# Performance work log

Hardware: AMD Instinct MI355X
Metric: run time of the kernel (lower is better)

The kernel has to match this reference:

```python
import jax, jax.numpy as jnp
import numpy as np

N, D, DFF, E, K = 2048, 1024, 4096, 8, 2  # tokens, d_model, d_ff, num_expert, top_k


def setup_inputs() -> dict:
    key = jax.random.key(0)
    ks = jax.random.split(key, 5)
    s = 0.02  # init scale
    return {
        "moe_inp": jax.random.normal(ks[0], (N, D), jnp.float32),
        "Wg": jax.random.normal(ks[1], (D, E), jnp.float32) * s,   # gate linear
        "bg": jnp.zeros((E,), jnp.float32),
        "W1": jax.random.normal(ks[2], (E, D, DFF), jnp.float32) * s,  # htoh4 per expert
        "b1": jnp.zeros((E, DFF), jnp.float32),
        "W2": jax.random.normal(ks[3], (E, DFF, D), jnp.float32) * s,  # h4toh per expert
        "b2": jnp.zeros((E, D), jnp.float32),
    }


def reference(moe_inp, Wg, bg, W1, b1, W2, b2):
    # --- NaiveGate: top-k experts per token, softmax over selected logits ---
    logits = moe_inp @ Wg + bg                      # [N, E]
    top_val, top_idx = jax.lax.top_k(logits, K)     # [N, K]
    score = jax.nn.softmax(top_val, axis=-1)        # [N, K]

    # Dense combine weights c[n, e] = sum_j score[n, j] * 1{top_idx[n, j] == e}.
    # This is the mathematically exact equivalent of scatter -> grouped expert
    # GEMM -> gather -> score-weighted combine in fmoe.
    comb = jnp.einsum(
        "nke,nk->ne", jax.nn.one_hot(top_idx, E, dtype=moe_inp.dtype), score
    )                                               # [N, E]

    # --- per-expert FFN: relu(x W1 + b1) W2 + b2, masked-combined by comb ---
    h = jax.nn.relu(jnp.einsum("nd,edh->enh", moe_inp, W1) + b1[:, None, :])  # [E, N, DFF]
    out = jnp.einsum("enh,ehd,ne->nd", h, W2, comb) + comb @ b2               # [N, D]
    return out
```

## Files before the change

kernel.cpp:

```cpp
#include <hip/hip_runtime.h>
#include <hip/hip_bf16.h>
#include <cstdint>
#include <cstddef>

#define NTOKS  2048
#define DMODEL 1024
#define DFFN   4096
#define NEXP   8
#define TS128  40

typedef __attribute__((ext_vector_type(8))) short short8;
typedef __attribute__((ext_vector_type(4))) float f32x4;
typedef __attribute__((ext_vector_type(4))) unsigned short u16x4;
typedef __attribute__((ext_vector_type(8))) unsigned short u16x8;

static constexpr size_t alignup(size_t x) { return (x + 255) & ~(size_t)255; }
static constexpr size_t OFF_XB   = 0;
static constexpr size_t OFF_CNT  = alignup(OFF_XB + (size_t)(NTOKS + 1) * DMODEL * 2);
static constexpr size_t OFF_OFFS = OFF_CNT + 256;
static constexpr size_t OFF_TOKE = OFF_OFFS + 256;
static constexpr size_t OFF_TOKT = OFF_TOKE + (size_t)NTOKS * 2 * 4;
static constexpr size_t OFF_TOKS = OFF_TOKT + (size_t)NTOKS * 2 * 4;
static constexpr size_t OFF_TI2  = alignup(OFF_TOKS + (size_t)NTOKS * 2 * 4);
static constexpr size_t OFF_CAP  = alignup(OFF_TI2 + TS128 * 8);
static constexpr size_t OFF_H    = alignup(OFF_CAP + (size_t)NEXP * NTOKS * 4);
static constexpr size_t OFF_WBA  = alignup(OFF_H + (size_t)(NTOKS * 2 + 128) * DFFN * 2);
static constexpr size_t OFF_WBB  = alignup(OFF_WBA + (size_t)NEXP * DMODEL * DFFN * 2);
static constexpr size_t OFF_Y    = OFF_WBA;

__device__ inline unsigned short f2bf(float f) {
  __hip_bfloat16 h = __float2bfloat16(f);
  return __builtin_bit_cast(unsigned short, h);
}

__device__ inline void gload16(const void* g, void* l) {
  __builtin_amdgcn_global_load_lds((const __attribute__((address_space(1))) unsigned int*)g,
                                   (__attribute__((address_space(3))) unsigned int*)l, 16, 0, 0);
}


__device__ __forceinline__ void conv_body(const float* __restrict__ x,
                                          unsigned short* __restrict__ xb, int vb) {
  size_t base = ((size_t)vb * 256 + threadIdx.x) * 8;
  const size_t total = (size_t)(NTOKS + 1) * DMODEL;
  if (base >= total) return;
  u16x8 o;
  if (base < (size_t)NTOKS * DMODEL) {
    f32x4 a = *(const f32x4*)(x + base);
    f32x4 b = *(const f32x4*)(x + base + 4);
#pragma unroll
    for (int j = 0; j < 4; ++j) { o[j] = f2bf(a[j]); o[4 + j] = f2bf(b[j]); }
  } else {
#pragma unroll
    for (int j = 0; j < 8; ++j) o[j] = 0;
  }
  *(u16x8*)(xb + base) = o;
}

template <int R, int C>
__device__ __forceinline__ void tc_body(const float* __restrict__ W,
                                        unsigned short* __restrict__ WT,
                                        int bx, int by, int bz,
                                        unsigned short (*T)[66]) {
  const int e = bz;
  const int c0 = bx * 64, r0 = by * 64;
  const float* Wp = W + (size_t)e * R * C;
  unsigned short* Tp = WT + (size_t)e * R * C;
  const int tid = threadIdx.x;
  const int rr = tid >> 4, cc = (tid & 15) << 2;
#pragma unroll
  for (int i = 0; i < 4; ++i) {
    int r = rr + (i << 4);
    f32x4 v = *(const f32x4*)(Wp + (size_t)(r0 + r) * C + c0 + cc);
    T[r][cc]     = f2bf(v[0]);
    T[r][cc + 1] = f2bf(v[1]);
    T[r][cc + 2] = f2bf(v[2]);
    T[r][cc + 3] = f2bf(v[3]);
  }
  __syncthreads();
  const int c = tid >> 2, kc = (tid & 3) << 4;
  u16x8 o0, o1;
#pragma unroll
  for (int i = 0; i < 8; ++i) { o0[i] = T[kc + i][c]; o1[i] = T[kc + 8 + i][c]; }
  unsigned short* dst = Tp + (size_t)(c0 + c) * R + r0 + kc;
  *(u16x8*)(dst) = o0;
  *(u16x8*)(dst + 8) = o1;
}

__device__ __forceinline__ void gate_body(const float* __restrict__ x,
                                          const float* __restrict__ Wg,
                                          const float* __restrict__ bg,
                                          int* __restrict__ tok_e,
                                          float* __restrict__ tok_s, int vb) {
  const int w = threadIdx.x >> 6, lane = threadIdx.x & 63;
  const int n = vb * 4 + w;
  float acc[8];
#pragma unroll
  for (int e = 0; e < 8; ++e) acc[e] = 0.f;
  const float* xr = x + (size_t)n * DMODEL;
#pragma unroll 4
  for (int it = 0; it < DMODEL / 64; ++it) {
    int d = it * 64 + lane;
    float xv = xr[d];
    f32x4 w0 = *(const f32x4*)(Wg + d * 8);
    f32x4 w1 = *(const f32x4*)(Wg + d * 8 + 4);
#pragma unroll
    for (int j = 0; j < 4; ++j) { acc[j] += xv * w0[j]; acc[4 + j] += xv * w1[j]; }
  }
#pragma unroll
  for (int e = 0; e < 8; ++e)
#pragma unroll
    for (int off = 32; off; off >>= 1) acc[e] += __shfl_xor(acc[e], off, 64);
  if (lane == 0) {
    float l[8];
#pragma unroll
    for (int e = 0; e < 8; ++e) l[e] = acc[e] + bg[e];
    int i0 = 0; float v0 = l[0];
#pragma unroll
    for (int e = 1; e < 8; ++e) if (l[e] > v0) { v0 = l[e]; i0 = e; }
    int i1 = (i0 == 0) ? 1 : 0; float v1 = l[i1];
#pragma unroll
    for (int e = 0; e < 8; ++e) if (e != i0 && l[e] > v1) { v1 = l[e]; i1 = e; }
    float t = expf(v1 - v0);
    float inv = 1.f / (1.f + t);
    tok_e[2 * n] = i0; tok_e[2 * n + 1] = i1;
    tok_s[2 * n] = inv; tok_s[2 * n + 1] = t * inv;
  }
}

template <int KTOT, int NTOT, int BN, bool FIRST, int KSPLIT>
__device__ __forceinline__ void gemm_body(const unsigned short* __restrict__ Asrc,
                                          const unsigned short* __restrict__ Bsrc,
                                          const float* __restrict__ bias,
                                          const int* __restrict__ cnt,
                                          const int* __restrict__ offs,
                                          const int2* __restrict__ tinfo,
                                          const int* __restrict__ cap,
                                          unsigned short* __restrict__ hout,
                                          float* __restrict__ yout,
                                          int bx, int by, int bz, char* smem) {
  const int2 ti = tinfo[by];
  if (ti.x < 0) return;
  const int e = ti.x, t0 = ti.y;
  const int c = cnt[e];
  const int base = offs[e] + t0;
  const int n0 = bx * BN;
  constexpr int KCH = KTOT / KSPLIT;
  constexpr int NT = KCH / 32;
  const int kb = bz * KCH;

  const int tid = threadIdx.x, w = tid >> 6, lane = tid & 63;
  const int l15 = lane & 15, lq = lane >> 4;
  constexpr int MR = 4;
  constexpr int NR = BN / 32;
  constexpr int BR = BN / 64;
  const int wr = w >> 1, wc = w & 1;

  unsigned short (*As)[128 * 32] = (unsigned short (*)[128 * 32])smem;
  unsigned short (*Bs)[BN * 32]  = (unsigned short (*)[BN * 32])(smem + 2 * 128 * 32 * 2);

  const int rl = tid >> 2;
  const int sw = (((tid & 3) ^ (rl & 3) ^ ((rl >> 2) & 3)) << 3);
  const unsigned short* aptr[2];
#pragma unroll
  for (int r = 0; r < 2; ++r) {
    int row = r * 64 + rl;
    size_t gr;
    if constexpr (FIRST) gr = (size_t)((t0 + row < c) ? cap[e * NTOKS + t0 + row] : NTOKS);
    else                 gr = (size_t)(base + row);
    aptr[r] = Asrc + gr * (size_t)KTOT + kb + sw;
  }
  const unsigned short* Be = Bsrc + (size_t)e * ((size_t)KTOT * NTOT);
  const unsigned short* bptr[BR];
#pragma unroll
  for (int r = 0; r < BR; ++r)
    bptr[r] = Be + (size_t)(n0 + r * 64 + rl) * KTOT + kb + sw;

  auto stageA = [&](int k0, int b) {
#pragma unroll
    for (int r = 0; r < 2; ++r)
      gload16(aptr[r] + k0, &As[b][(r * 64 + w * 16) << 5]);
  };
  auto stageB = [&](int k0, int b) {
#pragma unroll
    for (int r = 0; r < BR; ++r)
      gload16(bptr[r] + k0, &Bs[b][(r * 64 + w * 16) << 5]);
  };

  f32x4 acc[MR][NR] = {};

  stageA(0, 0);
  stageB(0, 0);
  __syncthreads();

  int buf = 0;
  for (int t = 0; t < NT; ++t) {
    const int nxt = buf ^ 1;
    if (t + 1 < NT) { stageA((t + 1) * 32, nxt); stageB((t + 1) * 32, nxt); }

    short8 a[MR], b[NR];
    const int sw0 = ((lq ^ (l15 & 3) ^ ((l15 >> 2) & 3)) << 3);
#pragma unroll
    for (int m = 0; m < MR; ++m)
      a[m] = *(const short8*)&As[buf][((wr * 64 + m * 16 + l15) << 5) + sw0];
#pragma unroll
    for (int nn = 0; nn < NR; ++nn)
      b[nn] = *(const short8*)&Bs[buf][((wc * (BN / 2) + nn * 16 + l15) << 5) + sw0];
#pragma unroll
    for (int m = 0; m < MR; ++m)
#pragma unroll
      for (int nn = 0; nn < NR; ++nn)
        acc[m][nn] = __builtin_amdgcn_mfma_f32_16x16x32_bf16(a[m], b[nn], acc[m][nn], 0, 0, 0);

    __syncthreads();
    buf = nxt;
  }

  if constexpr (FIRST) {
    const float* be = bias + (size_t)e * NTOT;
#pragma unroll
    for (int m = 0; m < MR; ++m) {
#pragma unroll
      for (int q2 = 0; q2 < 4; ++q2) {
        int row = wr * 64 + m * 16 + lq * 4 + q2;
        if (t0 + row < c) {
          unsigned short* hr = hout + (size_t)(base + row) * NTOT;
#pragma unroll
          for (int nn = 0; nn < NR; ++nn) {
            int col = n0 + wc * (BN / 2) + nn * 16 + l15;
            float v = acc[m][nn][q2] + be[col];
            v = v > 0.f ? v : 0.f;
            hr[col] = f2bf(v);
          }
        }
      }
    }
  } else {
    float* yz = yout + (size_t)bz * NTOKS * 2 * DMODEL;
#pragma unroll
    for (int m = 0; m < MR; ++m) {
#pragma unroll
      for (int q2 = 0; q2 < 4; ++q2) {
        int row = wr * 64 + m * 16 + lq * 4 + q2;
        if (t0 + row < c) {
          float* yr = yz + (size_t)(base + row) * NTOT;
#pragma unroll
          for (int nn = 0; nn < NR; ++nn) {
            int col = n0 + wc * (BN / 2) + nn * 16 + l15;
            yr[col] = acc[m][nn][q2];
          }
        }
      }
    }
  }
}


__global__ __launch_bounds__(256) void k_phase1(const float* __restrict__ x,
                                                const float* __restrict__ Wg,
                                                const float* __restrict__ bg,
                                                const float* __restrict__ W1,
                                                unsigned short* __restrict__ xb,
                                                unsigned short* __restrict__ wbA,
                                                int* __restrict__ tok_e,
                                                float* __restrict__ tok_s) {
  __shared__ unsigned short T[64][66];
  constexpr int NTC1 = (DFFN / 64) * (DMODEL / 64) * NEXP;
  constexpr int NCV  = (int)(((size_t)(NTOKS + 1) * DMODEL / 8 + 255) / 256);
  const int b = blockIdx.x;
  if (b < NTC1) {
    const int bx = b & 63, by = (b >> 6) & 15, bz = b >> 10;
    tc_body<DMODEL, DFFN>(W1, wbA, bx, by, bz, T);
  } else if (b < NTC1 + NCV) {
    conv_body(x, xb, b - NTC1);
  } else {
    gate_body(x, Wg, bg, tok_e, tok_s, b - NTC1 - NCV);
  }
}

__global__ __launch_bounds__(512) void k_scan(const int* __restrict__ tok_e,
                                              int* __restrict__ cnt,
                                              int* __restrict__ offs,
                                              int* __restrict__ tok_t,
                                              int* __restrict__ cap,
                                              int2* __restrict__ ti128) {
  __shared__ int scnt[NEXP];
  const int w = threadIdx.x >> 6, lane = threadIdx.x & 63;
  if (w < NEXP) {
    const int e = w;
    int t = 0;
    for (int it = 0; it < (NTOKS * 2) / 64; ++it) {
      const int j = it * 64 + lane;
      const bool p = (tok_e[j] == e);
      const unsigned long long m = __ballot(p);
      const int pos = __popcll(m & ((1ull << lane) - 1ull));
      if (p) {
        cap[e * NTOKS + t + pos] = j >> 1;
        tok_t[j] = t + pos;
      }
      t += __popcll(m);
    }
    if (lane == 0) { scnt[e] = t; cnt[e] = t; }
  }
  __syncthreads();
  if (threadIdx.x == 0) {
    int s = 0;
#pragma unroll
    for (int e = 0; e < NEXP; ++e) { offs[e] = s; s += scnt[e]; }
    int b = 0;
    for (int e = 0; e < NEXP; ++e)
      for (int t = 0; t * 128 < scnt[e]; ++t) { ti128[b] = make_int2(e, t * 128); ++b; }
    for (; b < TS128; ++b) ti128[b] = make_int2(-1, 0);
  }
}

__global__ __launch_bounds__(256) void k_phase3(const unsigned short* __restrict__ xb,
                                                const unsigned short* __restrict__ wbA,
                                                const float* __restrict__ b1,
                                                const float* __restrict__ W2,
                                                unsigned short* __restrict__ wbB,
                                                const int* __restrict__ cnt,
                                                const int* __restrict__ offs,
                                                const int2* __restrict__ ti128,
                                                const int* __restrict__ cap,
                                                unsigned short* __restrict__ h) {
  __shared__ __align__(16) char smem[2 * 128 * 32 * 2 + 2 * 128 * 32 * 2];
  constexpr int NG1 = (DFFN / 128) * TS128;
  const int b = blockIdx.x;
  if (b < NG1) {
    gemm_body<DMODEL, DFFN, 128, true, 1>(xb, wbA, b1, cnt, offs, ti128, cap, h, nullptr,
                                          b & 31, b >> 5, 0, smem);
  } else {
    const int t = b - NG1;
    const int bx = t & 15, by = (t >> 4) & 63, bz = t >> 10;
    tc_body<DFFN, DMODEL>(W2, wbB, bx, by, bz, (unsigned short (*)[66])smem);
  }
}

template <int KTOT, int NTOT, int BN, bool FIRST, int KSPLIT>
__global__ __launch_bounds__(256) void k_gemm(const unsigned short* __restrict__ Asrc,
                                              const unsigned short* __restrict__ Bsrc,
                                              const float* __restrict__ bias,
                                              const int* __restrict__ cnt,
                                              const int* __restrict__ offs,
                                              const int2* __restrict__ tinfo,
                                              const int* __restrict__ cap,
                                              unsigned short* __restrict__ hout,
                                              float* __restrict__ yout) {
  __shared__ __align__(16) char smem[2 * 128 * 32 * 2 + 2 * BN * 32 * 2];
  gemm_body<KTOT, NTOT, BN, FIRST, KSPLIT>(Asrc, Bsrc, bias, cnt, offs, tinfo, cap,
                                           hout, yout, blockIdx.x, blockIdx.y, blockIdx.z, smem);
}

__global__ __launch_bounds__(256) void k_combine(const float* __restrict__ y,
                                                 const float* __restrict__ b2,
                                                 const int* __restrict__ tok_e,
                                                 const int* __restrict__ tok_t,
                                                 const float* __restrict__ tok_s,
                                                 const int* __restrict__ offs,
                                                 float* __restrict__ out) {
  const int n = blockIdx.x, t = threadIdx.x;
  const float* y1 = y + (size_t)NTOKS * 2 * DMODEL;
  const int e0 = tok_e[2 * n], e1 = tok_e[2 * n + 1];
  const int s0i = offs[e0] + tok_t[2 * n];
  const int s1i = offs[e1] + tok_t[2 * n + 1];
  const float sc0 = tok_s[2 * n], sc1 = tok_s[2 * n + 1];
  f32x4 v0 = *(const f32x4*)(y + (size_t)s0i * DMODEL + t * 4);
  f32x4 u0 = *(const f32x4*)(y1 + (size_t)s0i * DMODEL + t * 4);
  f32x4 v1 = *(const f32x4*)(y + (size_t)s1i * DMODEL + t * 4);
  f32x4 u1 = *(const f32x4*)(y1 + (size_t)s1i * DMODEL + t * 4);
  f32x4 c0 = *(const f32x4*)(b2 + (size_t)e0 * DMODEL + t * 4);
  f32x4 c1 = *(const f32x4*)(b2 + (size_t)e1 * DMODEL + t * 4);
  f32x4 r = sc0 * ((v0 + u0) + c0) + sc1 * ((v1 + u1) + c1);
  *(f32x4*)(out + (size_t)n * DMODEL + t * 4) = r;
}

extern "C" void kernel_launch(void* const* d_in, const int* in_sizes, int n_in,
                              void* d_out, int out_size, void* d_ws, size_t ws_size,
                              hipStream_t stream) {
  const float* x  = (const float*)d_in[0];
  const float* Wg = (const float*)d_in[1];
  const float* bg = (const float*)d_in[2];
  const float* W1 = (const float*)d_in[3];
  const float* b1 = (const float*)d_in[4];
  const float* W2 = (const float*)d_in[5];
  const float* b2 = (const float*)d_in[6];
  float* out = (float*)d_out;

  char* ws = (char*)d_ws;
  unsigned short* xb = (unsigned short*)(ws + OFF_XB);
  int*   cnt   = (int*)(ws + OFF_CNT);
  int*   offs  = (int*)(ws + OFF_OFFS);
  int*   tok_e = (int*)(ws + OFF_TOKE);
  int*   tok_t = (int*)(ws + OFF_TOKT);
  float* tok_s = (float*)(ws + OFF_TOKS);
  int2*  ti128 = (int2*)(ws + OFF_TI2);
  int*   cap   = (int*)(ws + OFF_CAP);
  unsigned short* h   = (unsigned short*)(ws + OFF_H);
  unsigned short* wbA = (unsigned short*)(ws + OFF_WBA);
  unsigned short* wbB = (unsigned short*)(ws + OFF_WBB);
  float* y = (float*)(ws + OFF_Y);

  constexpr int NTC1 = (DFFN / 64) * (DMODEL / 64) * NEXP;
  constexpr int NCV  = (int)(((size_t)(NTOKS + 1) * DMODEL / 8 + 255) / 256);
  constexpr int NGT  = NTOKS / 4;
  constexpr int NG1  = (DFFN / 128) * TS128;
  constexpr int NTC2 = (DMODEL / 64) * (DFFN / 64) * NEXP;

  k_phase1<<<NTC1 + NCV + NGT, 256, 0, stream>>>(x, Wg, bg, W1, xb, wbA, tok_e, tok_s);
  k_scan<<<1, 512, 0, stream>>>(tok_e, cnt, offs, tok_t, cap, ti128);
  k_phase3<<<NG1 + NTC2, 256, 0, stream>>>(xb, wbA, b1, W2, wbB, cnt, offs, ti128, cap, h);
  k_gemm<DFFN, DMODEL, 64, false, 2><<<dim3(DMODEL / 64, TS128, 2), 256, 0, stream>>>(
      h, wbB, nullptr, cnt, offs, ti128, cap, nullptr, y);
  k_combine<<<NTOKS, 256, 0, stream>>>(y, b2, tok_e, tok_t, tok_s, offs, out);
}
```

Baseline: 234.6 us.

## Fuse score-weighted combine into second GEMM epilogue via atomic adds

Drops the separate combine kernel and the fp32 intermediate y buffer. The second expert GEMM now scales each row by its routing score, adds the b2 bias and atomically accumulates into the zeroed output, with the per-slot score stored during the scan. The split-K of two is removed, which halves the grid of that GEMM and doubles its K loop, and a memset of the output is added. Atomic fp32 adds make the summation order nondeterministic and add atomic traffic, and the smaller grid may reduce occupancy.

```diff
diff --git a/kernel.cpp b/kernel.cpp
--- a/kernel.cpp
+++ b/kernel.cpp
@@ -19,14 +19,13 @@
 static constexpr size_t OFF_CNT  = alignup(OFF_XB + (size_t)(NTOKS + 1) * DMODEL * 2);
 static constexpr size_t OFF_OFFS = OFF_CNT + 256;
 static constexpr size_t OFF_TOKE = OFF_OFFS + 256;
-static constexpr size_t OFF_TOKT = OFF_TOKE + (size_t)NTOKS * 2 * 4;
-static constexpr size_t OFF_TOKS = OFF_TOKT + (size_t)NTOKS * 2 * 4;
+static constexpr size_t OFF_TOKS = OFF_TOKE + (size_t)NTOKS * 2 * 4;
 static constexpr size_t OFF_TI2  = alignup(OFF_TOKS + (size_t)NTOKS * 2 * 4);
 static constexpr size_t OFF_CAP  = alignup(OFF_TI2 + TS128 * 8);
-static constexpr size_t OFF_H    = alignup(OFF_CAP + (size_t)NEXP * NTOKS * 4);
+static constexpr size_t OFF_SSC  = alignup(OFF_CAP + (size_t)NEXP * NTOKS * 4);
+static constexpr size_t OFF_H    = alignup(OFF_SSC + (size_t)NEXP * NTOKS * 4);
 static constexpr size_t OFF_WBA  = alignup(OFF_H + (size_t)(NTOKS * 2 + 128) * DFFN * 2);
 static constexpr size_t OFF_WBB  = alignup(OFF_WBA + (size_t)NEXP * DMODEL * DFFN * 2);
-static constexpr size_t OFF_Y    = OFF_WBA;
 
 __device__ inline unsigned short f2bf(float f) {
   __hip_bfloat16 h = __float2bfloat16(f);
@@ -128,7 +127,7 @@
   }
 }
 
-template <int KTOT, int NTOT, int BN, bool FIRST, int KSPLIT>
+template <int KTOT, int NTOT, int BN, bool FIRST>
 __device__ __forceinline__ void gemm_body(const unsigned short* __restrict__ Asrc,
                                           const unsigned short* __restrict__ Bsrc,
                                           const float* __restrict__ bias,
@@ -136,18 +135,17 @@
                                           const int* __restrict__ offs,
                                           const int2* __restrict__ tinfo,
                                           const int* __restrict__ cap,
+                                          const float* __restrict__ sscale,
                                           unsigned short* __restrict__ hout,
-                                          float* __restrict__ yout,
-                                          int bx, int by, int bz, char* smem) {
+                                          float* __restrict__ outp,
+                                          int bx, int by, char* smem) {
   const int2 ti = tinfo[by];
   if (ti.x < 0) return;
   const int e = ti.x, t0 = ti.y;
   const int c = cnt[e];
   const int base = offs[e] + t0;
   const int n0 = bx * BN;
-  constexpr int KCH = KTOT / KSPLIT;
-  constexpr int NT = KCH / 32;
-  const int kb = bz * KCH;
+  constexpr int NT = KTOT / 32;
 
   const int tid = threadIdx.x, w = tid >> 6, lane = tid & 63;
   const int l15 = lane & 15, lq = lane >> 4;
@@ -168,13 +166,13 @@
     size_t gr;
     if constexpr (FIRST) gr = (size_t)((t0 + row < c) ? cap[e * NTOKS + t0 + row] : NTOKS);
     else                 gr = (size_t)(base + row);
-    aptr[r] = Asrc + gr * (size_t)KTOT + kb + sw;
+    aptr[r] = Asrc + gr * (size_t)KTOT + sw;
   }
   const unsigned short* Be = Bsrc + (size_t)e * ((size_t)KTOT * NTOT);
   const unsigned short* bptr[BR];
 #pragma unroll
   for (int r = 0; r < BR; ++r)
-    bptr[r] = Be + (size_t)(n0 + r * 64 + rl) * KTOT + kb + sw;
+    bptr[r] = Be + (size_t)(n0 + r * 64 + rl) * KTOT + sw;
 
   auto stageA = [&](int k0, int b) {
 #pragma unroll
@@ -236,18 +234,21 @@
       }
     }
   } else {
-    float* yz = yout + (size_t)bz * NTOKS * 2 * DMODEL;
+    const float* be = bias + (size_t)e * NTOT;
 #pragma unroll
     for (int m = 0; m < MR; ++m) {
 #pragma unroll
       for (int q2 = 0; q2 < 4; ++q2) {
         int row = wr * 64 + m * 16 + lq * 4 + q2;
         if (t0 + row < c) {
-          float* yr = yz + (size_t)(base + row) * NTOT;
+          const int si = e * NTOKS + t0 + row;
+          const int n = cap[si];
+          const float sc = sscale[si];
+          float* orow = outp + (size_t)n * NTOT;
 #pragma unroll
           for (int nn = 0; nn < NR; ++nn) {
             int col = n0 + wc * (BN / 2) + nn * 16 + l15;
-            yr[col] = acc[m][nn][q2];
+            atomicAdd(&orow[col], sc * (acc[m][nn][q2] + be[col]));
           }
         }
       }
@@ -279,10 +280,11 @@
 }
 
 __global__ __launch_bounds__(512) void k_scan(const int* __restrict__ tok_e,
+                                              const float* __restrict__ tok_s,
                                               int* __restrict__ cnt,
                                               int* __restrict__ offs,
-                                              int* __restrict__ tok_t,
                                               int* __restrict__ cap,
+                                              float* __restrict__ sscale,
                                               int2* __restrict__ ti128) {
   __shared__ int scnt[NEXP];
   const int w = threadIdx.x >> 6, lane = threadIdx.x & 63;
@@ -296,7 +298,7 @@
       const int pos = __popcll(m & ((1ull << lane) - 1ull));
       if (p) {
         cap[e * NTOKS + t + pos] = j >> 1;
-        tok_t[j] = t + pos;
+        sscale[e * NTOKS + t + pos] = tok_s[j];
       }
       t += __popcll(m);
     }
@@ -328,8 +330,8 @@
   constexpr int NG1 = (DFFN / 128) * TS128;
   const int b = blockIdx.x;
   if (b < NG1) {
-    gemm_body<DMODEL, DFFN, 128, true, 1>(xb, wbA, b1, cnt, offs, ti128, cap, h, nullptr,
-                                          b & 31, b >> 5, 0, smem);
+    gemm_body<DMODEL, DFFN, 128, true>(xb, wbA, b1, cnt, offs, ti128, cap, nullptr,
+                                       h, nullptr, b & 31, b >> 5, smem);
   } else {
     const int t = b - NG1;
     const int bx = t & 15, by = (t >> 4) & 63, bz = t >> 10;
@@ -337,42 +339,18 @@
   }
 }
 
-template <int KTOT, int NTOT, int BN, bool FIRST, int KSPLIT>
-__global__ __launch_bounds__(256) void k_gemm(const unsigned short* __restrict__ Asrc,
-                                              const unsigned short* __restrict__ Bsrc,
-                                              const float* __restrict__ bias,
-                                              const int* __restrict__ cnt,
-                                              const int* __restrict__ offs,
-                                              const int2* __restrict__ tinfo,
-                                              const int* __restrict__ cap,
-                                              unsigned short* __restrict__ hout,
-                                              float* __restrict__ yout) {
-  __shared__ __align__(16) char smem[2 * 128 * 32 * 2 + 2 * BN * 32 * 2];
-  gemm_body<KTOT, NTOT, BN, FIRST, KSPLIT>(Asrc, Bsrc, bias, cnt, offs, tinfo, cap,
-                                           hout, yout, blockIdx.x, blockIdx.y, blockIdx.z, smem);
-}
-
-__global__ __launch_bounds__(256) void k_combine(const float* __restrict__ y,
-                                                 const float* __restrict__ b2,
-                                                 const int* __restrict__ tok_e,
-                                                 const int* __restrict__ tok_t,
-                                                 const float* __restrict__ tok_s,
-                                                 const int* __restrict__ offs,
-                                                 float* __restrict__ out) {
-  const int n = blockIdx.x, t = threadIdx.x;
-  const float* y1 = y + (size_t)NTOKS * 2 * DMODEL;
-  const int e0 = tok_e[2 * n], e1 = tok_e[2 * n + 1];
-  const int s0i = offs[e0] + tok_t[2 * n];
-  const int s1i = offs[e1] + tok_t[2 * n + 1];
-  const float sc0 = tok_s[2 * n], sc1 = tok_s[2 * n + 1];
-  f32x4 v0 = *(const f32x4*)(y + (size_t)s0i * DMODEL + t * 4);
-  f32x4 u0 = *(const f32x4*)(y1 + (size_t)s0i * DMODEL + t * 4);
-  f32x4 v1 = *(const f32x4*)(y + (size_t)s1i * DMODEL + t * 4);
-  f32x4 u1 = *(const f32x4*)(y1 + (size_t)s1i * DMODEL + t * 4);
-  f32x4 c0 = *(const f32x4*)(b2 + (size_t)e0 * DMODEL + t * 4);
-  f32x4 c1 = *(const f32x4*)(b2 + (size_t)e1 * DMODEL + t * 4);
-  f32x4 r = sc0 * ((v0 + u0) + c0) + sc1 * ((v1 + u1) + c1);
-  *(f32x4*)(out + (size_t)n * DMODEL + t * 4) = r;
+__global__ __launch_bounds__(256) void k_gemm2(const unsigned short* __restrict__ h,
+                                               const unsigned short* __restrict__ wbB,
+                                               const float* __restrict__ b2,
+                                               const int* __restrict__ cnt,
+                                               const int* __restrict__ offs,
+                                               const int2* __restrict__ ti128,
+                                               const int* __restrict__ cap,
+                                               const float* __restrict__ sscale,
+                                               float* __restrict__ out) {
+  __shared__ __align__(16) char smem[2 * 128 * 32 * 2 + 2 * 64 * 32 * 2];
+  gemm_body<DFFN, DMODEL, 64, false>(h, wbB, b2, cnt, offs, ti128, cap, sscale,
+                                     nullptr, out, blockIdx.x, blockIdx.y, smem);
 }
 
 extern "C" void kernel_launch(void* const* d_in, const int* in_sizes, int n_in,
@@ -392,14 +370,13 @@
   int*   cnt   = (int*)(ws + OFF_CNT);
   int*   offs  = (int*)(ws + OFF_OFFS);
   int*   tok_e = (int*)(ws + OFF_TOKE);
-  int*   tok_t = (int*)(ws + OFF_TOKT);
   float* tok_s = (float*)(ws + OFF_TOKS);
   int2*  ti128 = (int2*)(ws + OFF_TI2);
   int*   cap   = (int*)(ws + OFF_CAP);
+  float* sscale = (float*)(ws + OFF_SSC);
   unsigned short* h   = (unsigned short*)(ws + OFF_H);
   unsigned short* wbA = (unsigned short*)(ws + OFF_WBA);
   unsigned short* wbB = (unsigned short*)(ws + OFF_WBB);
-  float* y = (float*)(ws + OFF_Y);
 
   constexpr int NTC1 = (DFFN / 64) * (DMODEL / 64) * NEXP;
   constexpr int NCV  = (int)(((size_t)(NTOKS + 1) * DMODEL / 8 + 255) / 256);
@@ -407,10 +384,10 @@
   constexpr int NG1  = (DFFN / 128) * TS128;
   constexpr int NTC2 = (DMODEL / 64) * (DFFN / 64) * NEXP;
 
+  hipMemsetAsync(d_out, 0, (size_t)out_size * sizeof(float), stream);
   k_phase1<<<NTC1 + NCV + NGT, 256, 0, stream>>>(x, Wg, bg, W1, xb, wbA, tok_e, tok_s);
-  k_scan<<<1, 512, 0, stream>>>(tok_e, cnt, offs, tok_t, cap, ti128);
+  k_scan<<<1, 512, 0, stream>>>(tok_e, tok_s, cnt, offs, cap, sscale, ti128);
   k_phase3<<<NG1 + NTC2, 256, 0, stream>>>(xb, wbA, b1, W2, wbB, cnt, offs, ti128, cap, h);
-  k_gemm<DFFN, DMODEL, 64, false, 2><<<dim3(DMODEL / 64, TS128, 2), 256, 0, stream>>>(
-      h, wbB, nullptr, cnt, offs, ti128, cap, nullptr, y);
-  k_combine<<<NTOKS, 256, 0, stream>>>(y, b2, tok_e, tok_t, tok_s, offs, out);
-}
+  k_gemm2<<<dim3(DMODEL / 64, TS128), 256, 0, stream>>>(h, wbB, b2, cnt, offs, ti128,
+                                                        cap, sscale, out);
+}
```

Result: slower. 267.2 us (+13.9%).
